# Kernel optimization log

Hardware: AMD Instinct MI355X
Metric: run time of the kernel (lower is better)

The kernel has to match this reference:

```python
import jax, jax.numpy as jnp
import numpy as np

WIN = 8     # sliding-chunk window size (Long2DSCSelfAttention default w=8)
HEADS = 8   # num_heads


def setup_inputs() -> dict:
    key = jax.random.key(0)
    ks = jax.random.split(key, 3)
    B, C, H, W = 4, 512, 64, 64
    x = jax.random.normal(ks[0], (B, C, H, W), jnp.float32)
    w_qkv = jax.random.normal(ks[1], (3 * C, C), jnp.float32) * 0.02
    b_qkv = jnp.zeros((3 * C,), jnp.float32)
    w_proj = jax.random.normal(ks[2], (C, C), jnp.float32) * 0.02
    b_proj = jnp.zeros((C,), jnp.float32)
    return {"x": x, "w_qkv": w_qkv, "b_qkv": b_qkv, "w_proj": w_proj, "b_proj": b_proj}


def _chunk(t, nh, nw, win):
    B, _, _, h, d = t.shape
    t = t.reshape(B, nh, win, nw, win, h, d)
    return t.transpose(0, 5, 1, 3, 2, 4, 6).reshape(B, h, nh, nw, win * win, d)


def reference(x, w_qkv, b_qkv, w_proj, b_proj):
    B, C, H, W = x.shape
    win, heads = WIN, HEADS
    d = C // heads
    nh, nw = H // win, W // win
    m = win * win  # tokens per chunk

    xf = x.transpose(0, 2, 3, 1)                      # [B,H,W,C]
    qkv = xf @ w_qkv.T + b_qkv                        # [B,H,W,3C]
    qkv = qkv.reshape(B, H, W, 3, heads, d)
    q = _chunk(qkv[..., 0, :, :], nh, nw, win)        # [B,h,nh,nw,m,d]
    k = _chunk(qkv[..., 1, :, :], nh, nw, win)
    v = _chunk(qkv[..., 2, :, :], nh, nw, win)

    # pad chunk grid by one chunk on each side; gather 3x3 chunk neighborhoods
    kp = jnp.pad(k, ((0, 0), (0, 0), (1, 1), (1, 1), (0, 0), (0, 0)))
    vp = jnp.pad(v, ((0, 0), (0, 0), (1, 1), (1, 1), (0, 0), (0, 0)))
    k9 = jnp.concatenate([kp[:, :, i:i + nh, j:j + nw] for i in range(3) for j in range(3)], axis=4)  # [B,h,nh,nw,9m,d]
    v9 = jnp.concatenate([vp[:, :, i:i + nh, j:j + nw] for i in range(3) for j in range(3)], axis=4)

    # validity mask for neighbor chunks at the image boundary
    valid = jnp.pad(jnp.ones((nh, nw), bool), ((1, 1), (1, 1)))
    vmask = jnp.concatenate(
        [jnp.repeat(valid[i:i + nh, j:j + nw][..., None], m, axis=-1) for i in range(3) for j in range(3)],
        axis=-1)                                      # [nh,nw,9m]

    scale = float(d) ** -0.5
    attn = jnp.einsum('bhxyqd,bhxykd->bhxyqk', q * scale, k9)      # [B,h,nh,nw,m,9m]
    neg = jnp.asarray(-1e9, attn.dtype)
    attn = jnp.where(vmask[None, None, :, :, None, :], attn, neg)
    attn = jax.nn.softmax(attn, axis=-1)
    out = jnp.einsum('bhxyqk,bhxykd->bhxyqd', attn, v9)            # [B,h,nh,nw,m,d]

    out = out.reshape(B, heads, nh, nw, win, win, d)
    out = out.transpose(0, 2, 4, 3, 5, 1, 6).reshape(B, H, W, C)
    out = out @ w_proj.T + b_proj
    return out.transpose(0, 3, 1, 2)                               # [B,C,H,W]
```

## Files before the change

kernel.cpp:

```cpp
#include <hip/hip_runtime.h>
#include <cstdint>
#include <cstddef>

namespace {

constexpr int kC = 512;
constexpr int kHW = 4096;
constexpr int kHeads = 8;
constexpr int kChunkElems = 64 * 64;

typedef float f32x4 __attribute__((ext_vector_type(4)));
typedef __bf16 bf16x8 __attribute__((ext_vector_type(8)));
typedef _Float16 f16x8 __attribute__((ext_vector_type(8)));
union FragU { uint4 u; bf16x8 b; f16x8 h; };

__device__ __forceinline__ ushort bf16rn(float x) {
  uint u = __float_as_uint(x);
  return (ushort)((u + 0x7fffu + ((u >> 16) & 1u)) >> 16);
}
__device__ __forceinline__ ushort f16rn(float x) {
  _Float16 h = (_Float16)x;
  ushort u;
  __builtin_memcpy(&u, &h, 2);
  return u;
}
__device__ __forceinline__ void split2(float x, ushort& h, ushort& l) {
  ushort hh = bf16rn(x);
  float hf = __uint_as_float(((uint)hh) << 16);
  h = hh;
  l = bf16rn(x - hf);
}
__device__ __forceinline__ uint pack2(ushort a, ushort b) {
  return (uint)a | ((uint)b << 16);
}
__device__ __forceinline__ void gld16(const void* g, void* lds) {
  __builtin_amdgcn_global_load_lds(
      (const __attribute__((address_space(1))) uint32_t*)g,
      (__attribute__((address_space(3))) uint32_t*)lds, 16, 0, 0);
}

__global__ __launch_bounds__(256)
void convw_kernel(const float* __restrict__ w,
                  ushort* __restrict__ wh, ushort* __restrict__ wl)
{
  int idx = (blockIdx.x * 256 + threadIdx.x) * 8;
  float4 v0 = *(const float4*)(w + idx);
  float4 v1 = *(const float4*)(w + idx + 4);
  float xs[8] = {v0.x, v0.y, v0.z, v0.w, v1.x, v1.y, v1.z, v1.w};
  ushort hh[8], ll[8];
#pragma unroll
  for (int e = 0; e < 8; ++e) split2(xs[e], hh[e], ll[e]);
  *(uint4*)(wh + idx) = make_uint4(pack2(hh[0], hh[1]), pack2(hh[2], hh[3]),
                                   pack2(hh[4], hh[5]), pack2(hh[6], hh[7]));
  *(uint4*)(wl + idx) = make_uint4(pack2(ll[0], ll[1]), pack2(ll[2], ll[3]),
                                   pack2(ll[4], ll[5]), pack2(ll[6], ll[7]));
}

__global__ __launch_bounds__(256)
void convw16_kernel(const float* __restrict__ w, ushort* __restrict__ wh)
{
  int idx = (blockIdx.x * 256 + threadIdx.x) * 8;
  float4 v0 = *(const float4*)(w + idx);
  float4 v1 = *(const float4*)(w + idx + 4);
  float xs[8] = {v0.x, v0.y, v0.z, v0.w, v1.x, v1.y, v1.z, v1.w};
  ushort hh[8];
#pragma unroll
  for (int e = 0; e < 8; ++e) hh[e] = f16rn(xs[e]);
  *(uint4*)(wh + idx) = make_uint4(pack2(hh[0], hh[1]), pack2(hh[2], hh[3]),
                                   pack2(hh[4], hh[5]), pack2(hh[6], hh[7]));
}

__global__ __launch_bounds__(256)
void convx_kernel(const float* __restrict__ x, ushort* __restrict__ xt)
{
  __shared__ float LT[64][68];
  const int tid = threadIdx.x;
  const int t0 = blockIdx.x * 64;
  const int c0 = blockIdx.y * 64;
  const int b  = blockIdx.z;
  const float* xb = x + (size_t)b * kC * kHW;

#pragma unroll
  for (int u = 0; u < 4; ++u) {
    int idx = tid + u * 256;
    int rc = idx >> 4;
    int t4 = (idx & 15) << 2;
    float4 val = *(const float4*)(xb + (size_t)(c0 + rc) * kHW + t0 + t4);
    LT[t4 + 0][rc] = val.x;
    LT[t4 + 1][rc] = val.y;
    LT[t4 + 2][rc] = val.z;
    LT[t4 + 3][rc] = val.w;
  }
  __syncthreads();
#pragma unroll
  for (int u = 0; u < 4; ++u) {
    int idx = tid + u * 256;
    int rt = idx >> 4;
    int c4 = (idx & 15) << 2;
    float4 v = *(const float4*)&LT[rt][c4];
    size_t o = ((size_t)b * kHW + t0 + rt) * kC + c0 + c4;
    *(ushort4*)(xt + o) = make_ushort4(f16rn(v.x), f16rn(v.y),
                                       f16rn(v.z), f16rn(v.w));
  }
}

__global__ __launch_bounds__(256)
void qkv_mfma_kernel(const ushort* __restrict__ xt,
                     const ushort* __restrict__ wq,
                     const float* __restrict__ bqkv,
                     ushort* __restrict__ qo, ushort* __restrict__ ko,
                     ushort* __restrict__ vo)
{
  __shared__ __align__(16) ushort As[128 * 64];
  __shared__ __align__(16) ushort Bs[128 * 64];

  const int tid  = threadIdx.x;
  const int lane = tid & 63;
  const int wv   = tid >> 6;
  const int quad = lane >> 4;
  const int l15  = lane & 15;
  const int wm = wv & 1, wn = wv >> 1;
  const int m0 = blockIdx.x * 128;
  const int n0 = blockIdx.y * 128;
  const int b  = blockIdx.z;

  const ushort* xb = xt + (size_t)b * kHW * kC;

  f32x4 acc[4][4];
#pragma unroll
  for (int i = 0; i < 4; ++i)
#pragma unroll
    for (int j = 0; j < 4; ++j) acc[i][j] = (f32x4){0.f, 0.f, 0.f, 0.f};

  for (int k0 = 0; k0 < kC; k0 += 64) {
    __syncthreads();
#pragma unroll
    for (int ii = 0; ii < 4; ++ii) {
      int i = wv * 4 + ii;
      int m = i * 8 + (lane >> 3);
      int gch = (lane & 7) ^ (m & 7);
      size_t goA = (size_t)(m0 + m) * kC + k0 + gch * 8;
      gld16(xb + goA, (char*)As + i * 1024);
      size_t goB = (size_t)(n0 + m) * kC + k0 + gch * 8;
      gld16(wq + goB, (char*)Bs + i * 1024);
    }
    __syncthreads();

#pragma unroll
    for (int s = 0; s < 2; ++s) {
      const int gq = s * 4 + quad;
      FragU aA[4], bB[4];
#pragma unroll
      for (int mi = 0; mi < 4; ++mi) {
        int mr = wm * 64 + mi * 16 + l15;
        int off = mr * 64 + ((gq ^ (mr & 7)) * 8);
        aA[mi].u = *(const uint4*)&As[off];
      }
#pragma unroll
      for (int ni = 0; ni < 4; ++ni) {
        int nr = wn * 64 + ni * 16 + l15;
        int off = nr * 64 + ((gq ^ (nr & 7)) * 8);
        bB[ni].u = *(const uint4*)&Bs[off];
      }
#pragma unroll
      for (int mi = 0; mi < 4; ++mi)
#pragma unroll
        for (int ni = 0; ni < 4; ++ni)
          acc[mi][ni] = __builtin_amdgcn_mfma_f32_16x16x32_f16(aA[mi].h, bB[ni].h, acc[mi][ni], 0, 0, 0);
    }
  }

  const int sec = n0 >> 9;
  const int jwbase = n0 + wn * 64;
  const int head = (jwbase >> 6) & 7;
  const size_t hbb = ((size_t)b * kHeads + head) * 64;
  float biasv[4];
#pragma unroll
  for (int ni = 0; ni < 4; ++ni) biasv[ni] = bqkv[jwbase + ni * 16 + l15];

  if (sec == 2) {
#pragma unroll
    for (int ni = 0; ni < 4; ++ni) {
      int dd = ni * 16 + l15;
#pragma unroll
      for (int mi = 0; mi < 4; ++mi) {
        int t0t = m0 + wm * 64 + mi * 16 + quad * 4;
        int h = t0t >> 6, w = t0t & 63;
        int cy = h >> 3, iy = h & 7, cx = w >> 3, ix = w & 7;
        size_t cb = (hbb + cy * 8 + cx) * (size_t)kChunkElems;
        int tokb = iy * 8 + ix;
        ushort hh[4];
#pragma unroll
        for (int r = 0; r < 4; ++r) hh[r] = f16rn(acc[mi][ni][r] + biasv[ni]);
        *(ushort4*)(vo + cb + (size_t)dd * 64 + tokb) = make_ushort4(hh[0], hh[1], hh[2], hh[3]);
      }
    }
  } else {
    __syncthreads();
    ushort* dst = (sec == 0) ? qo : ko;
    const float sc = (sec == 0) ? 0.125f : 1.0f;
    ushort* tH = As + wv * 1152;
    const int ltok = lane >> 2;
    const int dd0 = (lane & 3) * 16;
#pragma unroll
    for (int mi = 0; mi < 4; ++mi) {
#pragma unroll
      for (int ni = 0; ni < 4; ++ni)
#pragma unroll
        for (int r = 0; r < 4; ++r)
          tH[(quad * 4 + r) * 68 + ni * 16 + l15] =
              f16rn((acc[mi][ni][r] + biasv[ni]) * sc);
      int tg = m0 + wm * 64 + mi * 16 + ltok;
      int h = tg >> 6, w = tg & 63;
      int cy = h >> 3, iy = h & 7, cx = w >> 3, ix = w & 7;
      size_t cb = (hbb + cy * 8 + cx) * (size_t)kChunkElems
                + (size_t)(iy * 8 + ix) * 64 + dd0;
      uint4 h0 = *(const uint4*)&tH[ltok * 68 + dd0];
      uint4 h1 = *(const uint4*)&tH[ltok * 68 + dd0 + 8];
      *(uint4*)(dst + cb) = h0;
      *(uint4*)(dst + cb + 8) = h1;
    }
  }
}

__global__ __launch_bounds__(256)
void attn_mfma_kernel(const ushort* __restrict__ qg, const ushort* __restrict__ kg,
                      const ushort* __restrict__ vg,
                      ushort* __restrict__ aoh, ushort* __restrict__ aol)
{
  __shared__ __align__(16) ushort KB[2][4096], VB[2][4096];
  __shared__ __align__(16) ushort Ps[4 * 16 * 72];

  const int tid  = threadIdx.x;
  const int lane = tid & 63;
  const int wv   = tid >> 6;
  const int quad = lane >> 4;
  const int l15  = lane & 15;

  const int bx = blockIdx.x;
  const int g  = (bx & 7) * 4 + ((bx >> 3) >> 6);
  const int c  = (bx >> 3) & 63;
  const int b = g >> 3, head = g & 7;
  const int cy = c >> 3, cx = c & 7;

  const size_t hb = (size_t)b * kHeads + head;
  const size_t cbase = (hb * 64 + cy * 8 + cx) * (size_t)kChunkElems;

  FragU aQ0, aQ1;
  {
    const ushort* qr = qg + cbase + (size_t)(wv * 16 + l15) * 64 + quad * 8;
    aQ0.u = *(const uint4*)(qr);
    aQ1.u = *(const uint4*)(qr + 32);
  }

  const int boff = ((lane >> 3) * 64) + (((lane & 7) ^ (lane >> 3)) * 8);
  ushort* PsW = Ps + wv * 1152;

  auto stage = [&](int buf, size_t nb) {
#pragma unroll
    for (int ii = 0; ii < 2; ++ii) {
      int ikb = wv * 2 + ii;
      size_t go = nb + (size_t)ikb * 512 + boff;
      gld16(kg + go, (char*)&KB[buf][0] + ikb * 1024);
      gld16(vg + go, (char*)&VB[buf][0] + ikb * 1024);
    }
  };
  auto nvalid = [&](int t) -> bool {
    int ny = cy + t / 3 - 1, nx = cx + t % 3 - 1;
    return (unsigned)ny < 8u && (unsigned)nx < 8u;
  };
  auto nbase = [&](int t) -> size_t {
    int ny = cy + t / 3 - 1, nx = cx + t % 3 - 1;
    return (hb * 64 + ny * 8 + nx) * (size_t)kChunkElems;
  };

  f32x4 o[4];
#pragma unroll
  for (int r = 0; r < 4; ++r) o[r] = (f32x4){0.f, 0.f, 0.f, 0.f};
  float rsum = 0.f;

  int t = 0;
  while (!nvalid(t)) ++t;
  stage(0, nbase(t));
  int cur = 0;

  for (;;) {
    int tn = t + 1;
    while (tn < 9 && !nvalid(tn)) ++tn;
    const bool more = (tn < 9);
    if (more) {
      stage(cur ^ 1, nbase(tn));
      asm volatile("s_waitcnt vmcnt(4)" ::: "memory");
    } else {
      asm volatile("s_waitcnt vmcnt(0)" ::: "memory");
    }
    asm volatile("s_barrier" ::: "memory");

    const ushort* KBc = &KB[cur][0];
    const ushort* VBc = &VB[cur][0];

    f32x4 s[4];
#pragma unroll
    for (int nt = 0; nt < 4; ++nt) s[nt] = (f32x4){0.f, 0.f, 0.f, 0.f};
#pragma unroll
    for (int nt = 0; nt < 4; ++nt) {
      int row = nt * 16 + l15;
      int sw = l15 & 7;
      int off0 = row * 64 + ((quad ^ sw) * 8);
      int off1 = row * 64 + (((4 + quad) ^ sw) * 8);
      FragU k0, k1;
      k0.u = *(const uint4*)&KBc[off0];
      k1.u = *(const uint4*)&KBc[off1];
      s[nt] = __builtin_amdgcn_mfma_f32_16x16x32_f16(k0.h, aQ0.h, s[nt], 0, 0, 0);
      s[nt] = __builtin_amdgcn_mfma_f32_16x16x32_f16(k1.h, aQ1.h, s[nt], 0, 0, 0);
    }

#pragma unroll
    for (int nt = 0; nt < 4; ++nt) {
      float e0 = __expf(s[nt][0]);
      float e1 = __expf(s[nt][1]);
      float e2 = __expf(s[nt][2]);
      float e3 = __expf(s[nt][3]);
      rsum += (e0 + e1) + (e2 + e3);
      *(ushort4*)&PsW[l15 * 72 + nt * 16 + quad * 4] =
          make_ushort4(f16rn(e0), f16rn(e1), f16rn(e2), f16rn(e3));
    }

    FragU aP0, aP1;
    aP0.u = *(const uint4*)&PsW[l15 * 72 + quad * 8];
    aP1.u = *(const uint4*)&PsW[l15 * 72 + 32 + quad * 8];

#pragma unroll
    for (int nt = 0; nt < 4; ++nt) {
      int row = nt * 16 + l15;
      int sw = l15 & 7;
      int off0 = row * 64 + ((quad ^ sw) * 8);
      int off1 = row * 64 + (((4 + quad) ^ sw) * 8);
      FragU v0, v1;
      v0.u = *(const uint4*)&VBc[off0];
      v1.u = *(const uint4*)&VBc[off1];
      o[nt] = __builtin_amdgcn_mfma_f32_16x16x32_f16(v0.h, aP0.h, o[nt], 0, 0, 0);
      o[nt] = __builtin_amdgcn_mfma_f32_16x16x32_f16(v1.h, aP1.h, o[nt], 0, 0, 0);
    }

    if (!more) break;
    asm volatile("s_barrier" ::: "memory");
    cur ^= 1;
    t = tn;
  }

  rsum += __shfl_xor(rsum, 16, 64);
  rsum += __shfl_xor(rsum, 32, 64);
  const float inv = 1.0f / rsum;

  const int trg = wv * 16 + l15;
  const int hp = cy * 8 + (trg >> 3);
  const int wp = cx * 8 + (trg & 7);
  const size_t obase = ((size_t)b * kHW + hp * 64 + wp) * (size_t)kC + head * 64;

#pragma unroll
  for (int nt = 0; nt < 4; ++nt) {
    float v0 = o[nt][0] * inv;
    float v1 = o[nt][1] * inv;
    float v2 = o[nt][2] * inv;
    float v3 = o[nt][3] * inv;
    *(ushort4*)(aoh + obase + nt * 16 + quad * 4) =
        make_ushort4(bf16rn(v0), bf16rn(v1), bf16rn(v2), bf16rn(v3));
    ushort h0, l0, h1, l1, h2, l2, h3, l3;
    split2(v0, h0, l0); split2(v1, h1, l1);
    split2(v2, h2, l2); split2(v3, h3, l3);
    *(ushort4*)(aol + obase + nt * 16 + quad * 4) =
        make_ushort4(l0, l1, l2, l3);
  }
}

__global__ __launch_bounds__(256)
void proj_mfma_kernel(const ushort* __restrict__ aoh, const ushort* __restrict__ aol,
                      const ushort* __restrict__ wph, const ushort* __restrict__ wpl,
                      const float* __restrict__ bproj,
                      float* __restrict__ out)
{
  __shared__ __align__(16) ushort AsH[128 * 64], AsL[128 * 64];
  __shared__ __align__(16) ushort BsH[64 * 64],  BsL[64 * 64];

  const int tid  = threadIdx.x;
  const int lane = tid & 63;
  const int wv   = tid >> 6;
  const int quad = lane >> 4;
  const int l15  = lane & 15;
  const int wm = wv & 1, wn = wv >> 1;
  const int n0g = blockIdx.x * 64;
  const int m0  = blockIdx.y * 128;
  const int b   = n0g >> 12;
  const int tl0 = n0g & 4095;

  f32x4 acc[4][2];
#pragma unroll
  for (int i = 0; i < 4; ++i)
#pragma unroll
    for (int j = 0; j < 2; ++j) acc[i][j] = (f32x4){0.f, 0.f, 0.f, 0.f};

  for (int k0 = 0; k0 < kC; k0 += 64) {
    __syncthreads();
#pragma unroll
    for (int ii = 0; ii < 4; ++ii) {
      int i = wv * 4 + ii;
      int m = i * 8 + (lane >> 3);
      int gch = (lane & 7) ^ (m & 7);
      size_t goA = (size_t)(m0 + m) * kC + k0 + gch * 8;
      gld16(wph + goA, (char*)AsH + i * 1024);
      gld16(wpl + goA, (char*)AsL + i * 1024);
    }
#pragma unroll
    for (int ii = 0; ii < 2; ++ii) {
      int i = wv * 2 + ii;
      int m = i * 8 + (lane >> 3);
      int gch = (lane & 7) ^ (m & 7);
      size_t goB = (size_t)(n0g + m) * kC + k0 + gch * 8;
      gld16(aoh + goB, (char*)BsH + i * 1024);
      gld16(aol + goB, (char*)BsL + i * 1024);
    }
    __syncthreads();

#pragma unroll
    for (int s = 0; s < 2; ++s) {
      const int gq = s * 4 + quad;
      FragU aH[4], aL[4], bH[2], bL[2];
#pragma unroll
      for (int mi = 0; mi < 4; ++mi) {
        int mr = wm * 64 + mi * 16 + l15;
        int off = mr * 64 + ((gq ^ (mr & 7)) * 8);
        aH[mi].u = *(const uint4*)&AsH[off];
        aL[mi].u = *(const uint4*)&AsL[off];
      }
#pragma unroll
      for (int ni = 0; ni < 2; ++ni) {
        int nr = wn * 32 + ni * 16 + l15;
        int off = nr * 64 + ((gq ^ (nr & 7)) * 8);
        bH[ni].u = *(const uint4*)&BsH[off];
        bL[ni].u = *(const uint4*)&BsL[off];
      }
#pragma unroll
      for (int mi = 0; mi < 4; ++mi)
#pragma unroll
        for (int ni = 0; ni < 2; ++ni) {
          acc[mi][ni] = __builtin_amdgcn_mfma_f32_16x16x32_bf16(aH[mi].b, bH[ni].b, acc[mi][ni], 0, 0, 0);
          acc[mi][ni] = __builtin_amdgcn_mfma_f32_16x16x32_bf16(aH[mi].b, bL[ni].b, acc[mi][ni], 0, 0, 0);
          acc[mi][ni] = __builtin_amdgcn_mfma_f32_16x16x32_bf16(aL[mi].b, bH[ni].b, acc[mi][ni], 0, 0, 0);
        }
    }
  }

#pragma unroll
  for (int mi = 0; mi < 4; ++mi)
#pragma unroll
    for (int r = 0; r < 4; ++r) {
      int c = m0 + wm * 64 + mi * 16 + quad * 4 + r;
      float bias = bproj[c];
      size_t rowb = ((size_t)b * kC + c) * (size_t)kHW + tl0 + wn * 32;
#pragma unroll
      for (int ni = 0; ni < 2; ++ni)
        out[rowb + ni * 16 + l15] = acc[mi][ni][r] + bias;
    }
}

}

extern "C" void kernel_launch(void* const* d_in, const int* in_sizes, int n_in,
                              void* d_out, int out_size, void* d_ws, size_t ws_size,
                              hipStream_t stream)
{
  const float* x     = (const float*)d_in[0];
  const float* wqkv  = (const float*)d_in[1];
  const float* bqkv  = (const float*)d_in[2];
  const float* wproj = (const float*)d_in[3];
  const float* bproj = (const float*)d_in[4];
  float* out = (float*)d_out;

  const size_t seg = (size_t)2048 * kChunkElems;
  ushort* base = (ushort*)d_ws;
  ushort* qb = base + 0 * seg;
  ushort* kb = base + 1 * seg;
  ushort* vb = base + 2 * seg;
  ushort* xt = base + 3 * seg;
  ushort* ao_hi = xt;
  ushort* ao_lo = base + 4 * seg;
  ushort* wqh = base + 5 * seg;
  ushort* wph = qb;
  ushort* wpl = qb + 262144;

  convw16_kernel<<<dim3(384), 256, 0, stream>>>(wqkv, wqh);
  convx_kernel<<<dim3(64, 8, 4), 256, 0, stream>>>(x, xt);
  qkv_mfma_kernel<<<dim3(32, 12, 4), 256, 0, stream>>>(xt, wqh, bqkv,
                                                       qb, kb, vb);
  attn_mfma_kernel<<<dim3(2048), 256, 0, stream>>>(qb, kb, vb, ao_hi, ao_lo);
  convw_kernel<<<dim3(128), 256, 0, stream>>>(wproj, wph, wpl);
  proj_mfma_kernel<<<dim3(256, 4), 256, 0, stream>>>(ao_hi, ao_lo, wph, wpl, bproj, out);
}
```

Before: 196.1 us.

## Single-buffer K/V tiles with staggered K and V prefetch in attention kernel

Replaces the double-buffered K/V shared-memory tiles with single buffers, loads K fragments into registers, then prefetches the next K tile while QK and softmax run, and prefetches the next V tile after PV finishes. This halves LDS use per block, which may allow more resident blocks per CU. In exchange it adds barriers, and the V load is exposed at the top of each iteration, so latency hiding between neighbor chunks is reduced.

```diff
diff --git a/kernel.cpp b/kernel.cpp
--- a/kernel.cpp
+++ b/kernel.cpp
@@ -228,7 +228,7 @@
                       const ushort* __restrict__ vg,
                       ushort* __restrict__ aoh, ushort* __restrict__ aol)
 {
-  __shared__ __align__(16) ushort KB[2][4096], VB[2][4096];
+  __shared__ __align__(16) ushort KB[4096], VB[4096];
   __shared__ __align__(16) ushort Ps[4 * 16 * 72];
 
   const int tid  = threadIdx.x;
@@ -256,13 +256,20 @@
   const int boff = ((lane >> 3) * 64) + (((lane & 7) ^ (lane >> 3)) * 8);
   ushort* PsW = Ps + wv * 1152;
 
-  auto stage = [&](int buf, size_t nb) {
+  auto stageK = [&](size_t nb) {
 #pragma unroll
     for (int ii = 0; ii < 2; ++ii) {
       int ikb = wv * 2 + ii;
       size_t go = nb + (size_t)ikb * 512 + boff;
-      gld16(kg + go, (char*)&KB[buf][0] + ikb * 1024);
-      gld16(vg + go, (char*)&VB[buf][0] + ikb * 1024);
+      gld16(kg + go, (char*)KB + ikb * 1024);
+    }
+  };
+  auto stageV = [&](size_t nb) {
+#pragma unroll
+    for (int ii = 0; ii < 2; ++ii) {
+      int ikb = wv * 2 + ii;
+      size_t go = nb + (size_t)ikb * 512 + boff;
+      gld16(vg + go, (char*)VB + ikb * 1024);
     }
   };
   auto nvalid = [&](int t) -> bool {
@@ -281,38 +288,38 @@
 
   int t = 0;
   while (!nvalid(t)) ++t;
-  stage(0, nbase(t));
-  int cur = 0;
+  stageK(nbase(t));
+  stageV(nbase(t));
 
   for (;;) {
     int tn = t + 1;
     while (tn < 9 && !nvalid(tn)) ++tn;
     const bool more = (tn < 9);
-    if (more) {
-      stage(cur ^ 1, nbase(tn));
-      asm volatile("s_waitcnt vmcnt(4)" ::: "memory");
-    } else {
-      asm volatile("s_waitcnt vmcnt(0)" ::: "memory");
-    }
+
+    asm volatile("s_waitcnt vmcnt(2)" ::: "memory");
     asm volatile("s_barrier" ::: "memory");
 
-    const ushort* KBc = &KB[cur][0];
-    const ushort* VBc = &VB[cur][0];
-
-    f32x4 s[4];
-#pragma unroll
-    for (int nt = 0; nt < 4; ++nt) s[nt] = (f32x4){0.f, 0.f, 0.f, 0.f};
+    FragU kf[8];
 #pragma unroll
     for (int nt = 0; nt < 4; ++nt) {
       int row = nt * 16 + l15;
       int sw = l15 & 7;
-      int off0 = row * 64 + ((quad ^ sw) * 8);
-      int off1 = row * 64 + (((4 + quad) ^ sw) * 8);
-      FragU k0, k1;
-      k0.u = *(const uint4*)&KBc[off0];
-      k1.u = *(const uint4*)&KBc[off1];
-      s[nt] = __builtin_amdgcn_mfma_f32_16x16x32_f16(k0.h, aQ0.h, s[nt], 0, 0, 0);
-      s[nt] = __builtin_amdgcn_mfma_f32_16x16x32_f16(k1.h, aQ1.h, s[nt], 0, 0, 0);
+      kf[nt * 2].u     = *(const uint4*)&KB[row * 64 + ((quad ^ sw) * 8)];
+      kf[nt * 2 + 1].u = *(const uint4*)&KB[row * 64 + (((4 + quad) ^ sw) * 8)];
+    }
+    asm volatile("s_waitcnt lgkmcnt(0)" ::: "memory");
+    asm volatile("s_waitcnt vmcnt(0)" ::: "memory");
+    asm volatile("s_barrier" ::: "memory");
+
+    if (more) stageK(nbase(tn));
+
+    f32x4 s[4];
+#pragma unroll
+    for (int nt = 0; nt < 4; ++nt) s[nt] = (f32x4){0.f, 0.f, 0.f, 0.f};
+#pragma unroll
+    for (int nt = 0; nt < 4; ++nt) {
+      s[nt] = __builtin_amdgcn_mfma_f32_16x16x32_f16(kf[nt * 2].h, aQ0.h, s[nt], 0, 0, 0);
+      s[nt] = __builtin_amdgcn_mfma_f32_16x16x32_f16(kf[nt * 2 + 1].h, aQ1.h, s[nt], 0, 0, 0);
     }
 
 #pragma unroll
@@ -337,15 +344,16 @@
       int off0 = row * 64 + ((quad ^ sw) * 8);
       int off1 = row * 64 + (((4 + quad) ^ sw) * 8);
       FragU v0, v1;
-      v0.u = *(const uint4*)&VBc[off0];
-      v1.u = *(const uint4*)&VBc[off1];
+      v0.u = *(const uint4*)&VB[off0];
+      v1.u = *(const uint4*)&VB[off1];
       o[nt] = __builtin_amdgcn_mfma_f32_16x16x32_f16(v0.h, aP0.h, o[nt], 0, 0, 0);
       o[nt] = __builtin_amdgcn_mfma_f32_16x16x32_f16(v1.h, aP1.h, o[nt], 0, 0, 0);
     }
 
+    asm volatile("s_waitcnt lgkmcnt(0)" ::: "memory");
+    asm volatile("s_barrier" ::: "memory");
     if (!more) break;
-    asm volatile("s_barrier" ::: "memory");
-    cur ^= 1;
+    stageV(nbase(tn));
     t = tn;
   }
 
```

New measurement: 196.4 us. No clear change (+0.1%).
